# Kernel tuning notes

Measured on AMD Instinct MI355X. Metric: run time of the kernel, lower is better.

The kernel has to match this reference:

```python
import jax, jax.numpy as jnp
import numpy as np

B, S, HID = 2, 2048, 2048
H, G = 32, 8            # query heads, kv heads
D = HID // H            # head_dim = 64
QPG = H // G            # q heads per kv group = 4


def setup_inputs() -> dict:
    key = jax.random.key(0)
    ks = jax.random.split(key, 5)
    sc = 0.02
    return {
        "x": jax.random.normal(ks[0], (B, S, HID), jnp.float32),
        "Wq": jax.random.normal(ks[1], (HID, HID), jnp.float32) * sc,
        "bq": jnp.zeros((HID,), jnp.float32),
        "Wk": jax.random.normal(ks[2], (HID, G * D), jnp.float32) * sc,
        "bk": jnp.zeros((G * D,), jnp.float32),
        "Wv": jax.random.normal(ks[3], (HID, G * D), jnp.float32) * sc,
        "bv": jnp.zeros((G * D,), jnp.float32),
        "Wo": jax.random.normal(ks[4], (HID, HID), jnp.float32) * sc,
        "bo": jnp.zeros((HID,), jnp.float32),
    }


def reference(x, Wq, bq, Wk, bk, Wv, bv, Wo, bo):
    b, s, _ = x.shape
    # projections (weights stored as [in, out])
    q = (x @ Wq + bq).reshape(b, s, G, QPG, D)      # [b,s,g,p,d]
    k = (x @ Wk + bk).reshape(b, s, G, D)           # [b,s,g,d]
    v = (x @ Wv + bv).reshape(b, s, G, D)
    scale = 1.0 / jnp.sqrt(jnp.asarray(D, x.dtype))
    # grouped attention: repeat_interleave of K/V expressed as shared g axis
    scores = jnp.einsum('bsgpd,btgd->bgpst', q, k) * scale  # [b,g,p,s,t]
    w = jax.nn.softmax(scores, axis=-1)
    o = jnp.einsum('bgpst,btgd->bsgpd', w, v)               # [b,s,g,p,d]
    o = o.reshape(b, s, HID)
    return o @ Wo + bo
```

## Files before the change

kernel.cpp:

```cpp
#include <hip/hip_runtime.h>
#include <hip/hip_bf16.h>


typedef __attribute__((ext_vector_type(8))) short shortx8;
typedef __attribute__((ext_vector_type(4))) float floatx4;

#define SEQ 2048
#define QSC 0.1803368801111204f

#if __has_builtin(__builtin_amdgcn_exp2f)
#define EXP2F(x) __builtin_amdgcn_exp2f(x)
#else
#define EXP2F(x) __expf((x) * 0.6931471805599453f)
#endif

__device__ __forceinline__ unsigned short f2bf(float f) {
  union { float f; unsigned u; } a; a.f = f;
  unsigned u = a.u;
  u += 0x7fffu + ((u >> 16) & 1u);
  return (unsigned short)(u >> 16);
}
__device__ __forceinline__ unsigned pk2f(float lo, float hi) {
  union { float f; unsigned u; } a, b; a.f = lo; b.f = hi;
  return ((a.u + 0x8000u) >> 16) | (((b.u + 0x8000u) >> 16) << 16);
}

__device__ __forceinline__ void gload16(const unsigned short* g, unsigned short* l) {
  __builtin_amdgcn_global_load_lds((const __attribute__((address_space(1))) void*)g,
                                   (__attribute__((address_space(3))) void*)l, 16, 0, 0);
}

__global__ void cast_bf16_kernel(const float* __restrict__ x,
                                 unsigned short* __restrict__ out, int n) {
  int i = (blockIdx.x * blockDim.x + threadIdx.x) * 4;
  if (i < n) {
    float4 v = *(const float4*)(x + i);
    ushort4 o;
    o.x = f2bf(v.x); o.y = f2bf(v.y); o.z = f2bf(v.z); o.w = f2bf(v.w);
    *(ushort4*)(out + i) = o;
  }
}

__global__ void transpose_cast_kernel(const float* __restrict__ W,
                                      unsigned short* __restrict__ WT,
                                      int K, int N) {
  __shared__ float tile[32][33];
  int x = blockIdx.x * 32 + threadIdx.x;
  int y0 = blockIdx.y * 32;
  for (int i = 0; i < 32; i += 8)
    tile[threadIdx.y + i][threadIdx.x] = W[(size_t)(y0 + threadIdx.y + i) * N + x];
  __syncthreads();
  int nx = y0 + threadIdx.x;
  int ny = blockIdx.x * 32 + threadIdx.y;
  for (int i = 0; i < 32; i += 8)
    WT[(size_t)(ny + i) * K + nx] = f2bf(tile[threadIdx.x][threadIdx.y + i]);
}

__global__ void concat_bias_kernel(const float* __restrict__ bq,
                                   const float* __restrict__ bk,
                                   const float* __restrict__ bv,
                                   float* __restrict__ out) {
  int i = blockIdx.x * 256 + threadIdx.x;
  if (i < 2048) out[i] = bq[i];
  else if (i < 2560) out[i] = bk[i - 2048];
  else if (i < 3072) out[i] = bv[i - 2560];
}

template <int MODE>
__global__ __launch_bounds__(256) void gemm_bt(const unsigned short* __restrict__ A,
                                               const unsigned short* __restrict__ BT,
                                               const float* __restrict__ bias,
                                               void* __restrict__ Cout,
                                               unsigned short* __restrict__ Kbuf,
                                               unsigned short* __restrict__ Vt,
                                               int M, int N, int K) {
  __shared__ __align__(16) unsigned short As[128 * 64];
  __shared__ __align__(16) unsigned short Bs[128 * 64];
  const int m0 = blockIdx.x * 128, n0 = blockIdx.y * 128;
  const int tid = threadIdx.x;
  const int lane = tid & 63, wave = tid >> 6;
  const int l15 = lane & 15, quad = lane >> 4;
  const int wm = (wave & 1) * 64, wn = (wave >> 1) * 64;

  const int r8 = lane >> 3;
  const int clog = (lane & 7) ^ r8;
  const unsigned short* aSrc = A + (size_t)(m0 + wave * 32 + r8) * K + clog * 8;
  const unsigned short* bSrc = BT + (size_t)(n0 + wave * 32 + r8) * K + clog * 8;
  unsigned short* aDst = &As[wave * 2048];
  unsigned short* bDst = &Bs[wave * 2048];

  const int s = l15 & 7;
  int aoff[4], boff[4];
#pragma unroll
  for (int i = 0; i < 4; i++) aoff[i] = (wm + i * 16 + l15) * 64 + (quad ^ s) * 8;
#pragma unroll
  for (int j = 0; j < 4; j++) boff[j] = (wn + j * 16 + l15) * 64 + (quad ^ s) * 8;

  floatx4 acc[4][4];
#pragma unroll
  for (int i = 0; i < 4; i++)
#pragma unroll
    for (int j = 0; j < 4; j++)
#pragma unroll
      for (int r = 0; r < 4; r++) acc[i][j][r] = 0.f;

  for (int k0 = 0; k0 < K; k0 += 64) {
    __syncthreads();
#pragma unroll
    for (int j = 0; j < 4; j++) {
      gload16(aSrc + (size_t)j * 8 * K + k0, aDst + j * 512);
      gload16(bSrc + (size_t)j * 8 * K + k0, bDst + j * 512);
    }
    __syncthreads();
    {
      shortx8 af[4], bf[4];
#pragma unroll
      for (int i = 0; i < 4; i++) af[i] = *(const shortx8*)&As[aoff[i]];
#pragma unroll
      for (int j = 0; j < 4; j++) bf[j] = *(const shortx8*)&Bs[boff[j]];
#pragma unroll
      for (int i = 0; i < 4; i++)
#pragma unroll
        for (int j = 0; j < 4; j++)
          acc[i][j] = __builtin_amdgcn_mfma_f32_16x16x32_bf16(af[i], bf[j], acc[i][j], 0, 0, 0);
#pragma unroll
      for (int i = 0; i < 4; i++) af[i] = *(const shortx8*)&As[aoff[i] ^ 32];
#pragma unroll
      for (int j = 0; j < 4; j++) bf[j] = *(const shortx8*)&Bs[boff[j] ^ 32];
#pragma unroll
      for (int i = 0; i < 4; i++)
#pragma unroll
        for (int j = 0; j < 4; j++)
          acc[i][j] = __builtin_amdgcn_mfma_f32_16x16x32_bf16(af[i], bf[j], acc[i][j], 0, 0, 0);
    }
  }

#pragma unroll
  for (int i = 0; i < 4; i++) {
#pragma unroll
    for (int j = 0; j < 4; j++) {
      int col = n0 + wn + j * 16 + l15;
      float bv = bias[col];
#pragma unroll
      for (int r = 0; r < 4; r++) {
        int row = m0 + wm + i * 16 + quad * 4 + r;
        float v = acc[i][j][r] + bv;
        if (MODE == 0) {
          ((float*)Cout)[(size_t)row * N + col] = v;
        } else {
          if (col < 2048) {
            ((unsigned short*)Cout)[(size_t)row * 2048 + col] = f2bf(v * QSC);
          } else if (col < 2560) {
            Kbuf[(size_t)row * 512 + (col - 2048)] = f2bf(v);
          } else {
            int g = (col - 2560) >> 6, d = (col - 2560) & 63;
            int b = row >> 11, sidx = row & 2047;
            Vt[(size_t)(((g << 1) | b) * 64 + d) * 2048 + sidx] = f2bf(v);
          }
        }
      }
    }
  }
}

__global__ __launch_bounds__(256) void attn_kernel(const unsigned short* __restrict__ Qb,
                                                   const unsigned short* __restrict__ Kb,
                                                   const unsigned short* __restrict__ Vt,
                                                   unsigned short* __restrict__ O) {
  const int qt = blockIdx.x, h = blockIdx.y, b = blockIdx.z;
  const int g = h >> 2;
  const int tid = threadIdx.x;
  const int lane = tid & 63, wave = tid >> 6;
  const int l15 = lane & 15, quad = lane >> 4;

  __shared__ __align__(16) unsigned short Ks[64 * 64];
  __shared__ __align__(16) unsigned short Vs[64 * 64];
  __shared__ __align__(16) unsigned short Ps[4][32][72];

  const int qrowA = b * SEQ + qt * 128 + wave * 32 + l15;
  const unsigned short* qpA = Qb + (size_t)qrowA * 2048 + h * 64 + quad * 8;
  shortx8 qA0 = *(const shortx8*)qpA;
  shortx8 qA1 = *(const shortx8*)(qpA + 32);
  shortx8 qB0 = *(const shortx8*)(qpA + 16 * 2048);
  shortx8 qB1 = *(const shortx8*)(qpA + 16 * 2048 + 32);

  const int r8 = lane >> 3;
  const int clog = (lane & 7) ^ r8;
  const unsigned short* kSrc = Kb + ((size_t)b * SEQ + wave * 16 + r8) * 512 + g * 64 + clog * 8;
  const unsigned short* vSrc = Vt + ((size_t)(((g << 1) | b) * 64) + wave * 16 + r8) * 2048 + clog * 8;
  unsigned short* kDst = &Ks[wave * 1024];
  unsigned short* vDst = &Vs[wave * 1024];

  const int s = l15 & 7;
  int foff[4];
#pragma unroll
  for (int i = 0; i < 4; i++) foff[i] = (i * 16 + l15) * 64 + (quad ^ s) * 8;

  float lA = 0.f, lB = 0.f;
  floatx4 oA[4], oB[4];
#pragma unroll
  for (int nd = 0; nd < 4; nd++)
#pragma unroll
    for (int r = 0; r < 4; r++) { oA[nd][r] = 0.f; oB[nd][r] = 0.f; }

  for (int t0 = 0; t0 < SEQ; t0 += 64) {
    __syncthreads();
    gload16(kSrc + (size_t)t0 * 512, kDst);
    gload16(kSrc + (size_t)(t0 + 8) * 512, kDst + 512);
    gload16(vSrc + t0, vDst);
    gload16(vSrc + (size_t)8 * 2048 + t0, vDst + 512);
    __syncthreads();

    floatx4 sA[4], sB[4];
#pragma unroll
    for (int i = 0; i < 4; i++) {
      shortx8 kf0 = *(const shortx8*)&Ks[foff[i]];
      shortx8 kf1 = *(const shortx8*)&Ks[foff[i] ^ 32];
      floatx4 c = {0.f, 0.f, 0.f, 0.f};
      c = __builtin_amdgcn_mfma_f32_16x16x32_bf16(kf0, qA0, c, 0, 0, 0);
      c = __builtin_amdgcn_mfma_f32_16x16x32_bf16(kf1, qA1, c, 0, 0, 0);
      sA[i] = c;
      floatx4 d = {0.f, 0.f, 0.f, 0.f};
      d = __builtin_amdgcn_mfma_f32_16x16x32_bf16(kf0, qB0, d, 0, 0, 0);
      d = __builtin_amdgcn_mfma_f32_16x16x32_bf16(kf1, qB1, d, 0, 0, 0);
      sB[i] = d;
    }

#pragma unroll
    for (int i = 0; i < 4; i++) {
      float a0 = EXP2F(sA[i][0]), a1 = EXP2F(sA[i][1]);
      float a2 = EXP2F(sA[i][2]), a3 = EXP2F(sA[i][3]);
      lA += (a0 + a1) + (a2 + a3);
      uint2 wa; wa.x = pk2f(a0, a1); wa.y = pk2f(a2, a3);
      *(uint2*)&Ps[wave][l15][i * 16 + quad * 4] = wa;
      float b0 = EXP2F(sB[i][0]), b1 = EXP2F(sB[i][1]);
      float b2 = EXP2F(sB[i][2]), b3 = EXP2F(sB[i][3]);
      lB += (b0 + b1) + (b2 + b3);
      uint2 wb; wb.x = pk2f(b0, b1); wb.y = pk2f(b2, b3);
      *(uint2*)&Ps[wave][16 + l15][i * 16 + quad * 4] = wb;
    }

#pragma unroll
    for (int ks = 0; ks < 2; ks++) {
      shortx8 pA = *(const shortx8*)&Ps[wave][l15][ks * 32 + quad * 8];
      shortx8 pB = *(const shortx8*)&Ps[wave][16 + l15][ks * 32 + quad * 8];
#pragma unroll
      for (int nd = 0; nd < 4; nd++) {
        shortx8 vf = *(const shortx8*)&Vs[ks ? (foff[nd] ^ 32) : foff[nd]];
        oA[nd] = __builtin_amdgcn_mfma_f32_16x16x32_bf16(vf, pA, oA[nd], 0, 0, 0);
        oB[nd] = __builtin_amdgcn_mfma_f32_16x16x32_bf16(vf, pB, oB[nd], 0, 0, 0);
      }
    }
  }

  lA += __shfl_xor(lA, 16, 64); lA += __shfl_xor(lA, 32, 64);
  lB += __shfl_xor(lB, 16, 64); lB += __shfl_xor(lB, 32, 64);
  float iA = 1.f / lA, iB = 1.f / lB;
  unsigned short* oPtr = O + (size_t)qrowA * 2048 + h * 64 + quad * 4;
#pragma unroll
  for (int nd = 0; nd < 4; nd++) {
    uint2 w;
    w.x = (unsigned)f2bf(oA[nd][0] * iA) | ((unsigned)f2bf(oA[nd][1] * iA) << 16);
    w.y = (unsigned)f2bf(oA[nd][2] * iA) | ((unsigned)f2bf(oA[nd][3] * iA) << 16);
    *(uint2*)(oPtr + nd * 16) = w;
    uint2 v;
    v.x = (unsigned)f2bf(oB[nd][0] * iB) | ((unsigned)f2bf(oB[nd][1] * iB) << 16);
    v.y = (unsigned)f2bf(oB[nd][2] * iB) | ((unsigned)f2bf(oB[nd][3] * iB) << 16);
    *(uint2*)(oPtr + (size_t)16 * 2048 + nd * 16) = v;
  }
}

extern "C" void kernel_launch(void* const* d_in, const int* in_sizes, int n_in,
                              void* d_out, int out_size, void* d_ws, size_t ws_size,
                              hipStream_t stream) {
  const float* x  = (const float*)d_in[0];
  const float* Wq = (const float*)d_in[1];
  const float* bq = (const float*)d_in[2];
  const float* Wk = (const float*)d_in[3];
  const float* bk = (const float*)d_in[4];
  const float* Wv = (const float*)d_in[5];
  const float* bv = (const float*)d_in[6];
  const float* Wo = (const float*)d_in[7];
  const float* bo = (const float*)d_in[8];
  float* out = (float*)d_out;

  char* ws = (char*)d_ws;
  unsigned short* WTall = (unsigned short*)ws;
  unsigned short* WoT   = (unsigned short*)(ws + 12582912);
  float*          bqkv  = (float*)(ws + 20971520);
  unsigned short* xb    = (unsigned short*)(ws + 20987904);
  unsigned short* Qbuf  = (unsigned short*)(ws + 37765120);
  unsigned short* Kbuf  = (unsigned short*)(ws + 54542336);
  unsigned short* Vt    = (unsigned short*)(ws + 58736640);
  unsigned short* Og    = xb;

  cast_bf16_kernel<<<8192, 256, 0, stream>>>(x, xb, 4096 * 2048);

  dim3 tb(32, 8);
  transpose_cast_kernel<<<dim3(64, 64), tb, 0, stream>>>(Wq, WTall, 2048, 2048);
  transpose_cast_kernel<<<dim3(16, 64), tb, 0, stream>>>(Wk, WTall + 2048 * 2048, 2048, 512);
  transpose_cast_kernel<<<dim3(16, 64), tb, 0, stream>>>(Wv, WTall + 2560 * 2048, 2048, 512);
  transpose_cast_kernel<<<dim3(64, 64), tb, 0, stream>>>(Wo, WoT, 2048, 2048);
  concat_bias_kernel<<<12, 256, 0, stream>>>(bq, bk, bv, bqkv);

  gemm_bt<2><<<dim3(32, 24), 256, 0, stream>>>(xb, WTall, bqkv, Qbuf, Kbuf, Vt, 4096, 3072, 2048);

  attn_kernel<<<dim3(16, 32, 2), 256, 0, stream>>>(Qbuf, Kbuf, Vt, Og);

  gemm_bt<0><<<dim3(32, 16), 256, 0, stream>>>(Og, WoT, bo, out, nullptr, nullptr, 4096, 2048, 2048);
}
```

Baseline: 334.9 us.

## Merge weight transposes, fold Q scale into weights, MFMA row sums, swizzle P

Merges the four weight transpose-cast launches into one 3D-grid kernel and folds the softmax scale into Wq and bq, so the QKV GEMM epilogue no longer multiplies. In attention, the per-lane exp row-sum adds and the final cross-lane shuffles are replaced by an extra MFMA against a ones vector. The padded P tile becomes an XOR-swizzled unpadded layout to avoid LDS bank conflicts. The attention launch is also split into two half-head launches, which adds launch overhead and a serialization point.

```diff
diff --git a/kernel.cpp b/kernel.cpp
--- a/kernel.cpp
+++ b/kernel.cpp
@@ -41,9 +41,20 @@
   }
 }
 
-__global__ void transpose_cast_kernel(const float* __restrict__ W,
-                                      unsigned short* __restrict__ WT,
-                                      int K, int N) {
+__global__ void transpose_cast_all(const float* __restrict__ Wq,
+                                   const float* __restrict__ Wk,
+                                   const float* __restrict__ Wv,
+                                   const float* __restrict__ Wo,
+                                   unsigned short* __restrict__ WT,
+                                   unsigned short* __restrict__ WoT) {
+  const int z = blockIdx.z;
+  const float* W; unsigned short* D; int N; float sc = 1.f;
+  if (z == 0)      { W = Wq; D = WT;                N = 2048; sc = QSC; }
+  else if (z == 1) { W = Wk; D = WT + 2048 * 2048;  N = 512; }
+  else if (z == 2) { W = Wv; D = WT + 2560 * 2048;  N = 512; }
+  else             { W = Wo; D = WoT;               N = 2048; }
+  if (blockIdx.x * 32 >= N) return;
+
   __shared__ float tile[32][33];
   int x = blockIdx.x * 32 + threadIdx.x;
   int y0 = blockIdx.y * 32;
@@ -53,7 +64,7 @@
   int nx = y0 + threadIdx.x;
   int ny = blockIdx.x * 32 + threadIdx.y;
   for (int i = 0; i < 32; i += 8)
-    WT[(size_t)(ny + i) * K + nx] = f2bf(tile[threadIdx.x][threadIdx.y + i]);
+    D[(size_t)(ny + i) * 2048 + nx] = f2bf(tile[threadIdx.x][threadIdx.y + i] * sc);
 }
 
 __global__ void concat_bias_kernel(const float* __restrict__ bq,
@@ -61,7 +72,7 @@
                                    const float* __restrict__ bv,
                                    float* __restrict__ out) {
   int i = blockIdx.x * 256 + threadIdx.x;
-  if (i < 2048) out[i] = bq[i];
+  if (i < 2048) out[i] = bq[i] * QSC;
   else if (i < 2560) out[i] = bk[i - 2048];
   else if (i < 3072) out[i] = bv[i - 2560];
 }
@@ -149,7 +160,7 @@
           ((float*)Cout)[(size_t)row * N + col] = v;
         } else {
           if (col < 2048) {
-            ((unsigned short*)Cout)[(size_t)row * 2048 + col] = f2bf(v * QSC);
+            ((unsigned short*)Cout)[(size_t)row * 2048 + col] = f2bf(v);
           } else if (col < 2560) {
             Kbuf[(size_t)row * 512 + (col - 2048)] = f2bf(v);
           } else {
@@ -166,8 +177,9 @@
 __global__ __launch_bounds__(256) void attn_kernel(const unsigned short* __restrict__ Qb,
                                                    const unsigned short* __restrict__ Kb,
                                                    const unsigned short* __restrict__ Vt,
-                                                   unsigned short* __restrict__ O) {
-  const int qt = blockIdx.x, h = blockIdx.y, b = blockIdx.z;
+                                                   unsigned short* __restrict__ O,
+                                                   int h0) {
+  const int qt = blockIdx.x, h = h0 + blockIdx.y, b = blockIdx.z;
   const int g = h >> 2;
   const int tid = threadIdx.x;
   const int lane = tid & 63, wave = tid >> 6;
@@ -175,7 +187,7 @@
 
   __shared__ __align__(16) unsigned short Ks[64 * 64];
   __shared__ __align__(16) unsigned short Vs[64 * 64];
-  __shared__ __align__(16) unsigned short Ps[4][32][72];
+  __shared__ __align__(16) unsigned short Ps[4 * 32 * 64];
 
   const int qrowA = b * SEQ + qt * 128 + wave * 32 + l15;
   const unsigned short* qpA = Qb + (size_t)qrowA * 2048 + h * 64 + quad * 8;
@@ -196,12 +208,26 @@
 #pragma unroll
   for (int i = 0; i < 4; i++) foff[i] = (i * 16 + l15) * 64 + (quad ^ s) * 8;
 
-  float lA = 0.f, lB = 0.f;
-  floatx4 oA[4], oB[4];
+  const int pbaseA = wave * 2048 + l15 * 64;
+  const int pbaseB = pbaseA + 16 * 64;
+  int pw[4];
+#pragma unroll
+  for (int i = 0; i < 4; i++) pw[i] = (((i * 2 + (quad >> 1)) ^ s) * 8) + (quad & 1) * 4;
+  int pr[2];
+#pragma unroll
+  for (int ks = 0; ks < 2; ks++) pr[ks] = ((ks * 4 + quad) ^ s) * 8;
+
+  shortx8 ones;
+#pragma unroll
+  for (int j = 0; j < 8; j++) ones[j] = (short)0x3F80;
+
+  floatx4 oA[4], oB[4], lAacc, lBacc;
 #pragma unroll
   for (int nd = 0; nd < 4; nd++)
 #pragma unroll
     for (int r = 0; r < 4; r++) { oA[nd][r] = 0.f; oB[nd][r] = 0.f; }
+#pragma unroll
+  for (int r = 0; r < 4; r++) { lAacc[r] = 0.f; lBacc[r] = 0.f; }
 
   for (int t0 = 0; t0 < SEQ; t0 += 64) {
     __syncthreads();
@@ -230,32 +256,30 @@
     for (int i = 0; i < 4; i++) {
       float a0 = EXP2F(sA[i][0]), a1 = EXP2F(sA[i][1]);
       float a2 = EXP2F(sA[i][2]), a3 = EXP2F(sA[i][3]);
-      lA += (a0 + a1) + (a2 + a3);
       uint2 wa; wa.x = pk2f(a0, a1); wa.y = pk2f(a2, a3);
-      *(uint2*)&Ps[wave][l15][i * 16 + quad * 4] = wa;
+      *(uint2*)&Ps[pbaseA + pw[i]] = wa;
       float b0 = EXP2F(sB[i][0]), b1 = EXP2F(sB[i][1]);
       float b2 = EXP2F(sB[i][2]), b3 = EXP2F(sB[i][3]);
-      lB += (b0 + b1) + (b2 + b3);
       uint2 wb; wb.x = pk2f(b0, b1); wb.y = pk2f(b2, b3);
-      *(uint2*)&Ps[wave][16 + l15][i * 16 + quad * 4] = wb;
+      *(uint2*)&Ps[pbaseB + pw[i]] = wb;
     }
 
 #pragma unroll
     for (int ks = 0; ks < 2; ks++) {
-      shortx8 pA = *(const shortx8*)&Ps[wave][l15][ks * 32 + quad * 8];
-      shortx8 pB = *(const shortx8*)&Ps[wave][16 + l15][ks * 32 + quad * 8];
+      shortx8 pA = *(const shortx8*)&Ps[pbaseA + pr[ks]];
+      shortx8 pB = *(const shortx8*)&Ps[pbaseB + pr[ks]];
 #pragma unroll
       for (int nd = 0; nd < 4; nd++) {
         shortx8 vf = *(const shortx8*)&Vs[ks ? (foff[nd] ^ 32) : foff[nd]];
         oA[nd] = __builtin_amdgcn_mfma_f32_16x16x32_bf16(vf, pA, oA[nd], 0, 0, 0);
         oB[nd] = __builtin_amdgcn_mfma_f32_16x16x32_bf16(vf, pB, oB[nd], 0, 0, 0);
       }
-    }
-  }
-
-  lA += __shfl_xor(lA, 16, 64); lA += __shfl_xor(lA, 32, 64);
-  lB += __shfl_xor(lB, 16, 64); lB += __shfl_xor(lB, 32, 64);
-  float iA = 1.f / lA, iB = 1.f / lB;
+      lAacc = __builtin_amdgcn_mfma_f32_16x16x32_bf16(ones, pA, lAacc, 0, 0, 0);
+      lBacc = __builtin_amdgcn_mfma_f32_16x16x32_bf16(ones, pB, lBacc, 0, 0, 0);
+    }
+  }
+
+  float iA = 1.f / lAacc[0], iB = 1.f / lBacc[0];
   unsigned short* oPtr = O + (size_t)qrowA * 2048 + h * 64 + quad * 4;
 #pragma unroll
   for (int nd = 0; nd < 4; nd++) {
@@ -296,16 +320,13 @@
 
   cast_bf16_kernel<<<8192, 256, 0, stream>>>(x, xb, 4096 * 2048);
 
-  dim3 tb(32, 8);
-  transpose_cast_kernel<<<dim3(64, 64), tb, 0, stream>>>(Wq, WTall, 2048, 2048);
-  transpose_cast_kernel<<<dim3(16, 64), tb, 0, stream>>>(Wk, WTall + 2048 * 2048, 2048, 512);
-  transpose_cast_kernel<<<dim3(16, 64), tb, 0, stream>>>(Wv, WTall + 2560 * 2048, 2048, 512);
-  transpose_cast_kernel<<<dim3(64, 64), tb, 0, stream>>>(Wo, WoT, 2048, 2048);
+  transpose_cast_all<<<dim3(64, 64, 4), dim3(32, 8), 0, stream>>>(Wq, Wk, Wv, Wo, WTall, WoT);
   concat_bias_kernel<<<12, 256, 0, stream>>>(bq, bk, bv, bqkv);
 
   gemm_bt<2><<<dim3(32, 24), 256, 0, stream>>>(xb, WTall, bqkv, Qbuf, Kbuf, Vt, 4096, 3072, 2048);
 
-  attn_kernel<<<dim3(16, 32, 2), 256, 0, stream>>>(Qbuf, Kbuf, Vt, Og);
+  attn_kernel<<<dim3(16, 16, 2), 256, 0, stream>>>(Qbuf, Kbuf, Vt, Og, 0);
+  attn_kernel<<<dim3(16, 16, 2), 256, 0, stream>>>(Qbuf, Kbuf, Vt, Og, 16);
 
   gemm_bt<0><<<dim3(32, 16), 256, 0, stream>>>(Og, WoT, bo, out, nullptr, nullptr, 4096, 2048, 2048);
 }
```

Measured after the change: 337.7 us. Within noise of the previous version (+0.8%).
